# Performance work log

Measured on AMD Instinct MI355X. Metric: run time of the kernel, lower is better.

## Reference

```python
import jax, jax.numpy as jnp
import numpy as np

B, S, D, H = 4, 2048, 1024, 16
DH = D // H


def setup_inputs() -> dict:
    key = jax.random.key(0)
    k1, k2, k3, k4, k5 = jax.random.split(key, 5)
    X = jax.random.normal(k1, (B, S, D), dtype=jnp.float32)
    W1 = jax.random.normal(k2, (3 * D, D), dtype=jnp.float32) * 0.02
    b1 = jax.random.normal(k3, (3 * D,), dtype=jnp.float32) * 0.01
    W2 = jax.random.normal(k4, (D, D), dtype=jnp.float32) * 0.02
    b2 = jax.random.normal(k5, (D,), dtype=jnp.float32) * 0.01
    return {"X": X, "W1": W1, "b1": b1, "W2": W2, "b2": b2}


def reference(X, W1, b1, W2, b2):
    b, s, d = X.shape
    # fused QKV projection (nn.Linear: y = x @ W.T + b)
    Y = X @ W1.T + b1                                   # [B,S,3D]
    Q, K, V = jnp.split(Y, 3, axis=2)                   # each [B,S,D]
    # reshape(x): view (B,S,H,DH) then permute(0,2,3,1) -> [B,H,DH,S]
    q = Q.reshape(b, s, H, DH).transpose(0, 2, 3, 1)    # [B,H,DH,S]
    v = V.reshape(b, s, H, DH).transpose(0, 2, 3, 1)    # [B,H,DH,S]
    # reshape(x, k=True): permute(0,2,1,3) -> [B,H,S,DH]
    k = K.reshape(b, s, H, DH).transpose(0, 2, 1, 3)    # [B,H,S,DH]
    # w = q @ k / sqrt(q.size(-1)) ; note q.size(-1) == S in this layout
    w = jnp.einsum('bhds,bhse->bhde', q, k) / jnp.sqrt(jnp.asarray(s, X.dtype))  # [B,H,DH,DH]
    w = jax.nn.softmax(w, axis=-1)
    out = jnp.einsum('bhde,bhes->bhds', w, v)           # [B,H,DH,S]
    # cat(): raw contiguous view of [B,H,DH,S] into [B,S,H*DH] (memory-order reshape)
    out = out.reshape(b, s, H * DH)                     # [B,S,D]
    return out @ W2.T + b2
```

## Files before the change

### kernel.cpp

```cpp
#include <hip/hip_runtime.h>
#include <stdint.h>

#define B_ 4
#define S_ 2048
#define D_ 1024
#define H_ 16
#define DH_ 64
#define M_TOT (B_*S_)
#define N1_ (3*D_)
#define K_ D_
#define NCH 8

typedef __bf16 bf16_8 __attribute__((ext_vector_type(8)));
typedef float  f32x4  __attribute__((ext_vector_type(4)));
typedef unsigned short u16;

typedef __attribute__((address_space(1))) const void* gas_t;
typedef __attribute__((address_space(3))) void*       las_t;

__device__ __forceinline__ unsigned short f2bf(float f) {
    union { float f; unsigned u; } v; v.f = f;
    unsigned r = v.u + 0x7FFFu + ((v.u >> 16) & 1u);
    return (unsigned short)(r >> 16);
}

__device__ __forceinline__ void async_ld16(const void* g, void* l) {
    __builtin_amdgcn_global_load_lds((gas_t)g, (las_t)l, 16, 0, 0);
}

__global__ __launch_bounds__(256)
void cast_kernel(const float* __restrict__ X, const float* __restrict__ W1,
                 const float* __restrict__ W2, unsigned short* __restrict__ Xb,
                 unsigned short* __restrict__ W1b, unsigned short* __restrict__ W2b) {
    const int nX  = (M_TOT * K_) / 4;
    const int nW1 = (N1_ * K_) / 4;
    int i = blockIdx.x * 256 + threadIdx.x;
    const float4* src; unsigned short* dst; int j;
    if (i < nX)            { src = (const float4*)X;  dst = Xb;  j = i; }
    else if (i < nX + nW1) { src = (const float4*)W1; dst = W1b; j = i - nX; }
    else                   { src = (const float4*)W2; dst = W2b; j = i - nX - nW1; }
    float4 v = src[j];
    ushort4 o;
    o.x = f2bf(v.x); o.y = f2bf(v.y); o.z = f2bf(v.z); o.w = f2bf(v.w);
    ((ushort4*)dst)[j] = o;
}

template<int N, int NBX, bool OUT_BF16>
__global__ __launch_bounds__(256)
void gemm_bt(const unsigned short* __restrict__ A,
             const unsigned short* __restrict__ Bm,
             const float* __restrict__ bias,
             void* __restrict__ C, int K) {
    __shared__ unsigned short As[128 * 64];
    __shared__ unsigned short Bs[128 * 64];
    const int t    = threadIdx.x;
    const int wid  = t >> 6;
    const int lane = t & 63;
    const int lrow = lane & 15;
    const int lq   = lane >> 4;

    const int lid  = blockIdx.y * NBX + blockIdx.x;
    const int xcd  = lid & 7;
    const int slot = lid >> 3;
    const int by   = xcd * (gridDim.y >> 3) + slot / NBX;
    const int bx   = slot % NBX;
    const int m0   = by * 128;
    const int n0   = bx * 128;

    const int wm   = (wid >> 1) * 64;
    const int wn   = (wid & 1) * 64;

    f32x4 acc[4][4] = {};

    for (int k0 = 0; k0 < K; k0 += 64) {
#pragma unroll
        for (int p = 0; p < 4; p++) {
            const int c   = p * 256 + t;
            const int row = c >> 3;
            const int kb  = (c & 7) ^ (row & 7);
            async_ld16(A  + (size_t)(m0 + row) * K + k0 + kb * 8, (char*)As + c * 16);
            async_ld16(Bm + (size_t)(n0 + row) * K + k0 + kb * 8, (char*)Bs + c * 16);
        }
        __syncthreads();

#pragma unroll
        for (int ks = 0; ks < 2; ks++) {
            bf16_8 af[4], bfr[4];
#pragma unroll
            for (int mt = 0; mt < 4; mt++) {
                const int r  = wm + mt * 16 + lrow;
                const int kb = (ks * 4 + lq) ^ (r & 7);
                af[mt] = *(const bf16_8*)(As + (r * 8 + kb) * 8);
            }
#pragma unroll
            for (int nt = 0; nt < 4; nt++) {
                const int r  = wn + nt * 16 + lrow;
                const int kb = (ks * 4 + lq) ^ (r & 7);
                bfr[nt] = *(const bf16_8*)(Bs + (r * 8 + kb) * 8);
            }
#pragma unroll
            for (int mt = 0; mt < 4; mt++)
#pragma unroll
                for (int nt = 0; nt < 4; nt++)
                    acc[mt][nt] = __builtin_amdgcn_mfma_f32_16x16x32_bf16(af[mt], bfr[nt], acc[mt][nt], 0, 0, 0);
        }
        __syncthreads();
    }

#pragma unroll
    for (int nt = 0; nt < 4; nt++) {
        const int col = n0 + wn + nt * 16 + lrow;
        const float bv = bias[col];
#pragma unroll
        for (int mt = 0; mt < 4; mt++) {
            const int row = m0 + wm + mt * 16 + lq * 4;
            f32x4 a = acc[mt][nt];
            if (OUT_BF16) {
                unsigned short* Cp = (unsigned short*)C;
#pragma unroll
                for (int i = 0; i < 4; i++)
                    Cp[(size_t)(row + i) * N + col] = f2bf(a[i] + bv);
            } else {
                float* Cp = (float*)C;
#pragma unroll
                for (int i = 0; i < 4; i++)
                    Cp[(size_t)(row + i) * N + col] = a[i] + bv;
            }
        }
    }
}


#define LDA_H(AS, MH, AF) do {                                                     \
  _Pragma("unroll") for (int m_ = 0; m_ < 4; m_++)                                 \
  _Pragma("unroll") for (int ks_ = 0; ks_ < 2; ks_++) {                            \
    const int rho_ = (MH)*128 + wr*64 + m_*16 + lrow;                              \
    AF[m_][ks_] = *(const bf16_8*)((const u16*)(AS) + rho_*64 +                    \
                                   (((ks_*4+lq) ^ (lrow&7)) << 3)); } } while (0)

#define LDB_H(BS, NH, BF) do {                                                     \
  _Pragma("unroll") for (int n_ = 0; n_ < 2; n_++)                                 \
  _Pragma("unroll") for (int ks_ = 0; ks_ < 2; ks_++) {                            \
    const int rho_ = (NH)*128 + wc*32 + n_*16 + lrow;                              \
    BF[n_][ks_] = *(const bf16_8*)((const u16*)(BS) + rho_*64 +                    \
                                   (((ks_*4+lq) ^ (lrow&7)) << 3)); } } while (0)

#define MMA_Q(MH, NH, AF, BF) do {                                                 \
    __builtin_amdgcn_s_setprio(1);                                                 \
    _Pragma("unroll") for (int ks_ = 0; ks_ < 2; ks_++)                            \
    _Pragma("unroll") for (int m_ = 0; m_ < 4; m_++)                               \
    _Pragma("unroll") for (int n_ = 0; n_ < 2; n_++)                               \
        acc[(MH)*4+m_][(NH)*2+n_] = __builtin_amdgcn_mfma_f32_16x16x32_bf16(       \
            AF[m_][ks_], BF[n_][ks_], acc[(MH)*4+m_][(NH)*2+n_], 0, 0, 0);         \
    __builtin_amdgcn_s_setprio(0);                                                 \
  } while (0)

#define BAR()       __builtin_amdgcn_s_barrier()
#define WAIT_LGKM() do { asm volatile("s_waitcnt lgkmcnt(0)" ::: "memory");        \
                         __builtin_amdgcn_sched_barrier(0); } while (0)

template<int N, int NBX, int KK, bool OUT_BF16>
__global__ __launch_bounds__(512, 1)
void gemm_bt2(const u16* __restrict__ A, const u16* __restrict__ Bm,
              const float* __restrict__ bias, void* __restrict__ C) {
    __shared__ u16 As[2][256 * 64];
    __shared__ u16 Bs[2][256 * 64];

    const int t    = threadIdx.x;
    const int wid  = t >> 6;
    const int lane = t & 63;
    const int lrow = lane & 15;
    const int lq   = lane >> 4;
    const int wr   = wid >> 2;
    const int wc   = wid & 3;

    const int lid  = blockIdx.y * NBX + blockIdx.x;
    const int xcd  = lid & 7;
    const int slot = lid >> 3;
    const int by   = xcd * (gridDim.y >> 3) + slot / NBX;
    const int bx   = slot % NBX;
    const int m0   = by * 256;
    const int n0   = bx * 256;

    const u16* Ab = A  + (size_t)m0 * KK;
    const u16* Bb = Bm + (size_t)n0 * KK;

    f32x4 acc[8][4] = {};

    auto STG = [&](const u16* __restrict__ G, char* lds, int half, int k0, bool isA) {
#pragma unroll
        for (int cc = 0; cc < 2; cc++) {
            const int rho = half * 128 + cc * 64 + (t >> 3);
            const int blk = t & 7;
            const int g   = isA ? (((rho >> 6) & 1) * 128 + ((rho >> 7) & 1) * 64 + (rho & 63))
                                : (((rho >> 5) & 3) * 64  + ((rho >> 7) & 1) * 32 + (rho & 31));
            async_ld16(G + (size_t)g * KK + k0 + ((blk ^ (rho & 7)) << 3),
                       lds + rho * 128 + blk * 16);
        }
    };

    char* as0 = (char*)&As[0][0]; char* as1 = (char*)&As[1][0];
    char* bs0 = (char*)&Bs[0][0]; char* bs1 = (char*)&Bs[1][0];

    STG(Ab, as0, 0, 0,  true);
    STG(Bb, bs0, 0, 0,  false);
    STG(Bb, bs0, 1, 0,  false);
    STG(Ab, as0, 1, 0,  true);
    STG(Ab, as1, 0, 64, true);
    STG(Bb, bs1, 0, 64, false);
    STG(Bb, bs1, 1, 64, false);
    asm volatile("s_waitcnt vmcnt(6)" ::: "memory");
    BAR();

    bf16_8 af[4][2], blo[2][2], bhi[2][2];

    constexpr int NT = KK / 64;
    constexpr int NI = NT / 2;

    for (int i = 0; i < NI; ++i) {
        const bool pf = (i < NI - 1);
        const int kE = (2 * i + 2) * 64;
        const int kO = (2 * i + 3) * 64;

        LDA_H(as0, 0, af);
        LDB_H(bs0, 0, blo);
        STG(Ab, as1, 1, (2 * i + 1) * 64, true);
        BAR(); WAIT_LGKM();
        MMA_Q(0, 0, af, blo);
        BAR();
        LDB_H(bs0, 1, bhi);
        if (pf) STG(Ab, as0, 0, kE, true);
        BAR(); WAIT_LGKM();
        MMA_Q(0, 1, af, bhi);
        BAR();
        LDA_H(as0, 1, af);
        if (pf) STG(Bb, bs0, 0, kE, false);
        BAR(); WAIT_LGKM();
        MMA_Q(1, 1, af, bhi);
        BAR();
        if (pf) STG(Bb, bs0, 1, kE, false);
        BAR();
        MMA_Q(1, 0, af, blo);
        if (pf) { asm volatile("s_waitcnt vmcnt(6)" ::: "memory"); }
        else    { asm volatile("s_waitcnt vmcnt(0)" ::: "memory"); }
        BAR();
        LDA_H(as1, 0, af);
        LDB_H(bs1, 0, blo);
        if (pf) STG(Ab, as0, 1, kE, true);
        BAR(); WAIT_LGKM();
        MMA_Q(0, 0, af, blo);
        BAR();
        LDB_H(bs1, 1, bhi);
        if (pf) STG(Ab, as1, 0, kO, true);
        BAR(); WAIT_LGKM();
        MMA_Q(0, 1, af, bhi);
        BAR();
        LDA_H(as1, 1, af);
        if (pf) STG(Bb, bs1, 0, kO, false);
        BAR(); WAIT_LGKM();
        MMA_Q(1, 1, af, bhi);
        BAR();
        if (pf) STG(Bb, bs1, 1, kO, false);
        BAR();
        MMA_Q(1, 0, af, blo);
        if (pf) asm volatile("s_waitcnt vmcnt(6)" ::: "memory");
        BAR();
    }

#pragma unroll
    for (int nt = 0; nt < 4; nt++) {
        const int col = n0 + wc * 64 + nt * 16 + lrow;
        const float bv = bias[col];
#pragma unroll
        for (int mt = 0; mt < 8; mt++) {
            const int row = m0 + wr * 128 + mt * 16 + lq * 4;
            f32x4 a = acc[mt][nt];
            if (OUT_BF16) {
                u16* Cp = (u16*)C;
#pragma unroll
                for (int i2 = 0; i2 < 4; i2++)
                    Cp[(size_t)(row + i2) * N + col] = f2bf(a[i2] + bv);
            } else {
                float* Cp = (float*)C;
#pragma unroll
                for (int i2 = 0; i2 < 4; i2++)
                    Cp[(size_t)(row + i2) * N + col] = a[i2] + bv;
            }
        }
    }
}

__global__ __launch_bounds__(256)
void attn_scores(const unsigned short* __restrict__ Y, float* __restrict__ Scp) {
    __shared__ unsigned short Qs[64 * 72];
    __shared__ unsigned short Ks[64 * 72];
    const int bh = blockIdx.x, ch = blockIdx.y;
    const int b = bh >> 4, h = bh & 15;
    const size_t ybase = (size_t)b * S_ * 3072;
    const int qoff = h * 64, koff = D_ + h * 64;
    const int t = threadIdx.x, wid = t >> 6, lane = t & 63;
    const int lrow = lane & 15, lq = lane >> 4;

    f32x4 acc[4] = {};
    const int sbeg = ch * (S_ / NCH);
    for (int s0 = sbeg; s0 < sbeg + S_ / NCH; s0 += 64) {
#pragma unroll
        for (int p = 0; p < 4; p++) {
            int idx = p * 256 + t;
            int r = idx >> 4, cg = (idx & 15) * 4;
            const size_t gb = ybase + (size_t)(s0 + r) * 3072;
            ushort4 q4 = *(const ushort4*)(Y + gb + qoff + cg);
            ushort4 k4 = *(const ushort4*)(Y + gb + koff + cg);
            Qs[(cg + 0) * 72 + r] = q4.x; Qs[(cg + 1) * 72 + r] = q4.y;
            Qs[(cg + 2) * 72 + r] = q4.z; Qs[(cg + 3) * 72 + r] = q4.w;
            Ks[(cg + 0) * 72 + r] = k4.x; Ks[(cg + 1) * 72 + r] = k4.y;
            Ks[(cg + 2) * 72 + r] = k4.z; Ks[(cg + 3) * 72 + r] = k4.w;
        }
        __syncthreads();
#pragma unroll
        for (int ks = 0; ks < 2; ks++) {
            bf16_8 aq = *(const bf16_8*)(Qs + (wid * 16 + lrow) * 72 + ks * 32 + lq * 8);
#pragma unroll
            for (int nt = 0; nt < 4; nt++) {
                bf16_8 bk = *(const bf16_8*)(Ks + (nt * 16 + lrow) * 72 + ks * 32 + lq * 8);
                acc[nt] = __builtin_amdgcn_mfma_f32_16x16x32_bf16(aq, bk, acc[nt], 0, 0, 0);
            }
        }
        __syncthreads();
    }

    float* out = Scp + (size_t)(bh * NCH + ch) * 64 * 64;
#pragma unroll
    for (int nt = 0; nt < 4; nt++)
#pragma unroll
        for (int i = 0; i < 4; i++)
            out[(wid * 16 + lq * 4 + i) * 64 + nt * 16 + lrow] = acc[nt][i];
}

__global__ __launch_bounds__(256)
void attn_softmax(const float* __restrict__ Scp, unsigned short* __restrict__ Wb) {
    const int bh = blockIdx.x;
    const int t = threadIdx.x;
    const int d = t >> 2, q = t & 3;
    float s[16] = {};
#pragma unroll
    for (int c = 0; c < NCH; c++) {
        const float4* p = (const float4*)(Scp + ((size_t)(bh * NCH + c) * 64 + d) * 64 + q * 16);
#pragma unroll
        for (int j = 0; j < 4; j++) {
            float4 v = p[j];
            s[j*4+0] += v.x; s[j*4+1] += v.y; s[j*4+2] += v.z; s[j*4+3] += v.w;
        }
    }
    const float scale = 0.022097086912079608f;
    float m = -3.0e38f;
#pragma unroll
    for (int i = 0; i < 16; i++) { s[i] *= scale; m = fmaxf(m, s[i]); }
    m = fmaxf(m, __shfl_xor(m, 1));
    m = fmaxf(m, __shfl_xor(m, 2));
    float sum = 0.f;
#pragma unroll
    for (int i = 0; i < 16; i++) { s[i] = __expf(s[i] - m); sum += s[i]; }
    sum += __shfl_xor(sum, 1);
    sum += __shfl_xor(sum, 2);
    const float inv = 1.0f / sum;
    unsigned short* w = Wb + (size_t)bh * 4096 + d * 64 + q * 16;
    ushort4 o0, o1, o2, o3;
    o0.x=f2bf(s[0]*inv);  o0.y=f2bf(s[1]*inv);  o0.z=f2bf(s[2]*inv);  o0.w=f2bf(s[3]*inv);
    o1.x=f2bf(s[4]*inv);  o1.y=f2bf(s[5]*inv);  o1.z=f2bf(s[6]*inv);  o1.w=f2bf(s[7]*inv);
    o2.x=f2bf(s[8]*inv);  o2.y=f2bf(s[9]*inv);  o2.z=f2bf(s[10]*inv); o2.w=f2bf(s[11]*inv);
    o3.x=f2bf(s[12]*inv); o3.y=f2bf(s[13]*inv); o3.z=f2bf(s[14]*inv); o3.w=f2bf(s[15]*inv);
    ((ushort4*)w)[0]=o0; ((ushort4*)w)[1]=o1; ((ushort4*)w)[2]=o2; ((ushort4*)w)[3]=o3;
}

__global__ __launch_bounds__(256)
void attn_out(const unsigned short* __restrict__ Y, const unsigned short* __restrict__ Wb,
              unsigned short* __restrict__ O) {
    __shared__ unsigned short Ws[64 * 72];
    const int bh = blockIdx.x, sc = blockIdx.y;
    const int b = bh >> 4, h = bh & 15;
    const size_t ybase = (size_t)b * S_ * 3072;
    const int voff = 2 * D_ + h * 64;
    const int t = threadIdx.x, wid = t >> 6, lane = t & 63;
    const int lrow = lane & 15, lq = lane >> 4;

    {
        const int d = t >> 2, q = t & 3;
        const uint4* src = (const uint4*)(Wb + (size_t)bh * 4096 + d * 64 + q * 16);
        uint4* dst = (uint4*)(Ws + d * 72 + q * 16);
        dst[0] = src[0];
        *(uint4*)(Ws + d * 72 + q * 16 + 8) = src[1];
    }
    __syncthreads();

    bf16_8 aw[4][2];
#pragma unroll
    for (int mt = 0; mt < 4; mt++)
#pragma unroll
        for (int ks = 0; ks < 2; ks++)
            aw[mt][ks] = *(const bf16_8*)(Ws + (mt * 16 + lrow) * 72 + ks * 32 + lq * 8);

    const size_t obase = (size_t)b * (H_ * DH_ * S_) + (size_t)h * (DH_ * S_);
    const int s0 = sc * 256 + wid * 64;
    f32x4 o[4][4] = {};
#pragma unroll
    for (int ks = 0; ks < 2; ks++) {
        bf16_8 bv[4];
#pragma unroll
        for (int nt = 0; nt < 4; nt++)
            bv[nt] = *(const bf16_8*)(Y + ybase + (size_t)(s0 + nt * 16 + lrow) * 3072 + voff + ks * 32 + lq * 8);
#pragma unroll
        for (int mt = 0; mt < 4; mt++)
#pragma unroll
            for (int nt = 0; nt < 4; nt++)
                o[mt][nt] = __builtin_amdgcn_mfma_f32_16x16x32_bf16(aw[mt][ks], bv[nt], o[mt][nt], 0, 0, 0);
    }
#pragma unroll
    for (int mt = 0; mt < 4; mt++)
#pragma unroll
        for (int nt = 0; nt < 4; nt++) {
            const int d = mt * 16 + lq * 4;
            const int s = s0 + nt * 16 + lrow;
#pragma unroll
            for (int i = 0; i < 4; i++)
                O[obase + (size_t)(d + i) * S_ + s] = f2bf(o[mt][nt][i]);
        }
}

extern "C" void kernel_launch(void* const* d_in, const int* in_sizes, int n_in,
                              void* d_out, int out_size, void* d_ws, size_t ws_size,
                              hipStream_t stream) {
    const float* X  = (const float*)d_in[0];
    const float* W1 = (const float*)d_in[1];
    const float* b1 = (const float*)d_in[2];
    const float* W2 = (const float*)d_in[3];
    const float* b2 = (const float*)d_in[4];

    char* ws = (char*)d_ws;
    unsigned short* Xb  = (unsigned short*)(ws + 0);
    unsigned short* W1b = (unsigned short*)(ws + (16u << 20));
    unsigned short* W2b = (unsigned short*)(ws + (22u << 20));
    unsigned short* Yb  = (unsigned short*)(ws + (24u << 20));
    unsigned short* Wb  = (unsigned short*)(ws + 0);
    unsigned short* Ob  = (unsigned short*)(ws + (1u << 20));
    float* Scp = (float*)d_out;

    cast_kernel<<<12288, 256, 0, stream>>>(X, W1, W2, Xb, W1b, W2b);
    gemm_bt2<N1_, N1_/256, K_, true><<<dim3(N1_ / 256, M_TOT / 256), 512, 0, stream>>>(Xb, W1b, b1, Yb);
    attn_scores<<<dim3(64, NCH), 256, 0, stream>>>(Yb, Scp);
    attn_softmax<<<64, 256, 0, stream>>>(Scp, Wb);
    attn_out<<<dim3(64, NCH), 256, 0, stream>>>(Yb, Wb, Ob);
    gemm_bt<D_, D_/128, false><<<dim3(D_ / 128, M_TOT / 128), 256, 0, stream>>>(Ob, W2b, b2, d_out, K_);
}
```

Measured before the change: 221.9 us.

## Shrink QKV GEMM tile to 256x128 and fuse softmax into attention output

The QKV projection GEMM tile shrinks from 256x256 to 256x128. Each of 8 waves now owns a 64x64 sub-tile, the B staging buffer is halved, and the vmcnt waits are adjusted to match. This doubles the block count from 384 to 768 to fill the GPU's compute units better, at the cost of lower arithmetic intensity per block. Separately, the softmax kernel is fused into the attention-output kernel: each block recomputes the 64x64 softmax straight into shared memory. That removes one launch and the bf16 weight round-trip, but repeats the partial-score reduction across the 8 sequence chunks.

```diff
diff --git a/kernel.cpp b/kernel.cpp
--- a/kernel.cpp
+++ b/kernel.cpp
@@ -132,26 +132,26 @@
 
 
 #define LDA_H(AS, MH, AF) do {                                                     \
-  _Pragma("unroll") for (int m_ = 0; m_ < 4; m_++)                                 \
+  _Pragma("unroll") for (int m_ = 0; m_ < 2; m_++)                                 \
   _Pragma("unroll") for (int ks_ = 0; ks_ < 2; ks_++) {                            \
-    const int rho_ = (MH)*128 + wr*64 + m_*16 + lrow;                              \
+    const int rho_ = (MH)*128 + wr*32 + m_*16 + lrow;                              \
     AF[m_][ks_] = *(const bf16_8*)((const u16*)(AS) + rho_*64 +                    \
                                    (((ks_*4+lq) ^ (lrow&7)) << 3)); } } while (0)
 
 #define LDB_H(BS, NH, BF) do {                                                     \
   _Pragma("unroll") for (int n_ = 0; n_ < 2; n_++)                                 \
   _Pragma("unroll") for (int ks_ = 0; ks_ < 2; ks_++) {                            \
-    const int rho_ = (NH)*128 + wc*32 + n_*16 + lrow;                              \
+    const int rho_ = (NH)*64 + wc*32 + n_*16 + lrow;                               \
     BF[n_][ks_] = *(const bf16_8*)((const u16*)(BS) + rho_*64 +                    \
                                    (((ks_*4+lq) ^ (lrow&7)) << 3)); } } while (0)
 
 #define MMA_Q(MH, NH, AF, BF) do {                                                 \
     __builtin_amdgcn_s_setprio(1);                                                 \
     _Pragma("unroll") for (int ks_ = 0; ks_ < 2; ks_++)                            \
-    _Pragma("unroll") for (int m_ = 0; m_ < 4; m_++)                               \
+    _Pragma("unroll") for (int m_ = 0; m_ < 2; m_++)                               \
     _Pragma("unroll") for (int n_ = 0; n_ < 2; n_++)                               \
-        acc[(MH)*4+m_][(NH)*2+n_] = __builtin_amdgcn_mfma_f32_16x16x32_bf16(       \
-            AF[m_][ks_], BF[n_][ks_], acc[(MH)*4+m_][(NH)*2+n_], 0, 0, 0);         \
+        acc[(MH)*2+m_][(NH)*2+n_] = __builtin_amdgcn_mfma_f32_16x16x32_bf16(       \
+            AF[m_][ks_], BF[n_][ks_], acc[(MH)*2+m_][(NH)*2+n_], 0, 0, 0);         \
     __builtin_amdgcn_s_setprio(0);                                                 \
   } while (0)
 
@@ -161,18 +161,18 @@
 
 template<int N, int NBX, int KK, bool OUT_BF16>
 __global__ __launch_bounds__(512, 1)
-void gemm_bt2(const u16* __restrict__ A, const u16* __restrict__ Bm,
+void gemm_bt3(const u16* __restrict__ A, const u16* __restrict__ Bm,
               const float* __restrict__ bias, void* __restrict__ C) {
     __shared__ u16 As[2][256 * 64];
-    __shared__ u16 Bs[2][256 * 64];
+    __shared__ u16 Bs[2][128 * 64];
 
     const int t    = threadIdx.x;
     const int wid  = t >> 6;
     const int lane = t & 63;
     const int lrow = lane & 15;
     const int lq   = lane >> 4;
-    const int wr   = wid >> 2;
-    const int wc   = wid & 3;
+    const int wr   = wid >> 1;
+    const int wc   = wid & 1;
 
     const int lid  = blockIdx.y * NBX + blockIdx.x;
     const int xcd  = lid & 7;
@@ -180,39 +180,45 @@
     const int by   = xcd * (gridDim.y >> 3) + slot / NBX;
     const int bx   = slot % NBX;
     const int m0   = by * 256;
-    const int n0   = bx * 256;
+    const int n0   = bx * 128;
 
     const u16* Ab = A  + (size_t)m0 * KK;
     const u16* Bb = Bm + (size_t)n0 * KK;
 
-    f32x4 acc[8][4] = {};
-
-    auto STG = [&](const u16* __restrict__ G, char* lds, int half, int k0, bool isA) {
+    f32x4 acc[4][4] = {};
+
+    auto STGA = [&](char* lds, int half, int k0) {
 #pragma unroll
         for (int cc = 0; cc < 2; cc++) {
             const int rho = half * 128 + cc * 64 + (t >> 3);
             const int blk = t & 7;
-            const int g   = isA ? (((rho >> 6) & 1) * 128 + ((rho >> 7) & 1) * 64 + (rho & 63))
-                                : (((rho >> 5) & 3) * 64  + ((rho >> 7) & 1) * 32 + (rho & 31));
-            async_ld16(G + (size_t)g * KK + k0 + ((blk ^ (rho & 7)) << 3),
+            const int g   = ((rho >> 5) & 3) * 64 + (rho >> 7) * 32 + (rho & 31);
+            async_ld16(Ab + (size_t)g * KK + k0 + ((blk ^ (rho & 7)) << 3),
                        lds + rho * 128 + blk * 16);
         }
+    };
+    auto STGB = [&](char* lds, int half, int k0) {
+        const int rho = half * 64 + (t >> 3);
+        const int blk = t & 7;
+        const int g   = ((rho >> 5) & 1) * 64 + (rho >> 6) * 32 + (rho & 31);
+        async_ld16(Bb + (size_t)g * KK + k0 + ((blk ^ (rho & 7)) << 3),
+                   lds + rho * 128 + blk * 16);
     };
 
     char* as0 = (char*)&As[0][0]; char* as1 = (char*)&As[1][0];
     char* bs0 = (char*)&Bs[0][0]; char* bs1 = (char*)&Bs[1][0];
 
-    STG(Ab, as0, 0, 0,  true);
-    STG(Bb, bs0, 0, 0,  false);
-    STG(Bb, bs0, 1, 0,  false);
-    STG(Ab, as0, 1, 0,  true);
-    STG(Ab, as1, 0, 64, true);
-    STG(Bb, bs1, 0, 64, false);
-    STG(Bb, bs1, 1, 64, false);
-    asm volatile("s_waitcnt vmcnt(6)" ::: "memory");
+    STGA(as0, 0, 0);
+    STGB(bs0, 0, 0);
+    STGB(bs0, 1, 0);
+    STGA(as0, 1, 0);
+    STGA(as1, 0, 64);
+    STGB(bs1, 0, 64);
+    STGB(bs1, 1, 64);
+    asm volatile("s_waitcnt vmcnt(4)" ::: "memory");
     BAR();
 
-    bf16_8 af[4][2], blo[2][2], bhi[2][2];
+    bf16_8 af[2][2], blo[2][2], bhi[2][2];
 
     constexpr int NT = KK / 64;
     constexpr int NI = NT / 2;
@@ -224,46 +230,46 @@
 
         LDA_H(as0, 0, af);
         LDB_H(bs0, 0, blo);
-        STG(Ab, as1, 1, (2 * i + 1) * 64, true);
+        STGA(as1, 1, (2 * i + 1) * 64);
         BAR(); WAIT_LGKM();
         MMA_Q(0, 0, af, blo);
         BAR();
         LDB_H(bs0, 1, bhi);
-        if (pf) STG(Ab, as0, 0, kE, true);
+        if (pf) STGA(as0, 0, kE);
         BAR(); WAIT_LGKM();
         MMA_Q(0, 1, af, bhi);
         BAR();
         LDA_H(as0, 1, af);
-        if (pf) STG(Bb, bs0, 0, kE, false);
+        if (pf) STGB(bs0, 0, kE);
         BAR(); WAIT_LGKM();
         MMA_Q(1, 1, af, bhi);
         BAR();
-        if (pf) STG(Bb, bs0, 1, kE, false);
+        if (pf) STGB(bs0, 1, kE);
         BAR();
         MMA_Q(1, 0, af, blo);
-        if (pf) { asm volatile("s_waitcnt vmcnt(6)" ::: "memory"); }
+        if (pf) { asm volatile("s_waitcnt vmcnt(4)" ::: "memory"); }
         else    { asm volatile("s_waitcnt vmcnt(0)" ::: "memory"); }
         BAR();
         LDA_H(as1, 0, af);
         LDB_H(bs1, 0, blo);
-        if (pf) STG(Ab, as0, 1, kE, true);
+        if (pf) STGA(as0, 1, kE);
         BAR(); WAIT_LGKM();
         MMA_Q(0, 0, af, blo);
         BAR();
         LDB_H(bs1, 1, bhi);
-        if (pf) STG(Ab, as1, 0, kO, true);
+        if (pf) STGA(as1, 0, kO);
         BAR(); WAIT_LGKM();
         MMA_Q(0, 1, af, bhi);
         BAR();
         LDA_H(as1, 1, af);
-        if (pf) STG(Bb, bs1, 0, kO, false);
+        if (pf) STGB(bs1, 0, kO);
         BAR(); WAIT_LGKM();
         MMA_Q(1, 1, af, bhi);
         BAR();
-        if (pf) STG(Bb, bs1, 1, kO, false);
+        if (pf) STGB(bs1, 1, kO);
         BAR();
         MMA_Q(1, 0, af, blo);
-        if (pf) asm volatile("s_waitcnt vmcnt(6)" ::: "memory");
+        if (pf) asm volatile("s_waitcnt vmcnt(4)" ::: "memory");
         BAR();
     }
 
@@ -272,8 +278,8 @@
         const int col = n0 + wc * 64 + nt * 16 + lrow;
         const float bv = bias[col];
 #pragma unroll
-        for (int mt = 0; mt < 8; mt++) {
-            const int row = m0 + wr * 128 + mt * 16 + lq * 4;
+        for (int mt = 0; mt < 4; mt++) {
+            const int row = m0 + wr * 64 + mt * 16 + lq * 4;
             f32x4 a = acc[mt][nt];
             if (OUT_BF16) {
                 u16* Cp = (u16*)C;
@@ -338,44 +344,9 @@
 }
 
 __global__ __launch_bounds__(256)
-void attn_softmax(const float* __restrict__ Scp, unsigned short* __restrict__ Wb) {
-    const int bh = blockIdx.x;
-    const int t = threadIdx.x;
-    const int d = t >> 2, q = t & 3;
-    float s[16] = {};
-#pragma unroll
-    for (int c = 0; c < NCH; c++) {
-        const float4* p = (const float4*)(Scp + ((size_t)(bh * NCH + c) * 64 + d) * 64 + q * 16);
-#pragma unroll
-        for (int j = 0; j < 4; j++) {
-            float4 v = p[j];
-            s[j*4+0] += v.x; s[j*4+1] += v.y; s[j*4+2] += v.z; s[j*4+3] += v.w;
-        }
-    }
-    const float scale = 0.022097086912079608f;
-    float m = -3.0e38f;
-#pragma unroll
-    for (int i = 0; i < 16; i++) { s[i] *= scale; m = fmaxf(m, s[i]); }
-    m = fmaxf(m, __shfl_xor(m, 1));
-    m = fmaxf(m, __shfl_xor(m, 2));
-    float sum = 0.f;
-#pragma unroll
-    for (int i = 0; i < 16; i++) { s[i] = __expf(s[i] - m); sum += s[i]; }
-    sum += __shfl_xor(sum, 1);
-    sum += __shfl_xor(sum, 2);
-    const float inv = 1.0f / sum;
-    unsigned short* w = Wb + (size_t)bh * 4096 + d * 64 + q * 16;
-    ushort4 o0, o1, o2, o3;
-    o0.x=f2bf(s[0]*inv);  o0.y=f2bf(s[1]*inv);  o0.z=f2bf(s[2]*inv);  o0.w=f2bf(s[3]*inv);
-    o1.x=f2bf(s[4]*inv);  o1.y=f2bf(s[5]*inv);  o1.z=f2bf(s[6]*inv);  o1.w=f2bf(s[7]*inv);
-    o2.x=f2bf(s[8]*inv);  o2.y=f2bf(s[9]*inv);  o2.z=f2bf(s[10]*inv); o2.w=f2bf(s[11]*inv);
-    o3.x=f2bf(s[12]*inv); o3.y=f2bf(s[13]*inv); o3.z=f2bf(s[14]*inv); o3.w=f2bf(s[15]*inv);
-    ((ushort4*)w)[0]=o0; ((ushort4*)w)[1]=o1; ((ushort4*)w)[2]=o2; ((ushort4*)w)[3]=o3;
-}
-
-__global__ __launch_bounds__(256)
-void attn_out(const unsigned short* __restrict__ Y, const unsigned short* __restrict__ Wb,
-              unsigned short* __restrict__ O) {
+void attn_out_fused(const unsigned short* __restrict__ Y,
+                    const float* __restrict__ Scp,
+                    unsigned short* __restrict__ O) {
     __shared__ unsigned short Ws[64 * 72];
     const int bh = blockIdx.x, sc = blockIdx.y;
     const int b = bh >> 4, h = bh & 15;
@@ -386,10 +357,31 @@
 
     {
         const int d = t >> 2, q = t & 3;
-        const uint4* src = (const uint4*)(Wb + (size_t)bh * 4096 + d * 64 + q * 16);
-        uint4* dst = (uint4*)(Ws + d * 72 + q * 16);
-        dst[0] = src[0];
-        *(uint4*)(Ws + d * 72 + q * 16 + 8) = src[1];
+        float s[16] = {};
+#pragma unroll
+        for (int c = 0; c < NCH; c++) {
+            const float4* p = (const float4*)(Scp + ((size_t)(bh * NCH + c) * 64 + d) * 64 + q * 16);
+#pragma unroll
+            for (int j = 0; j < 4; j++) {
+                float4 v = p[j];
+                s[j*4+0] += v.x; s[j*4+1] += v.y; s[j*4+2] += v.z; s[j*4+3] += v.w;
+            }
+        }
+        const float scale = 0.022097086912079608f;
+        float m = -3.0e38f;
+#pragma unroll
+        for (int i = 0; i < 16; i++) { s[i] *= scale; m = fmaxf(m, s[i]); }
+        m = fmaxf(m, __shfl_xor(m, 1));
+        m = fmaxf(m, __shfl_xor(m, 2));
+        float sum = 0.f;
+#pragma unroll
+        for (int i = 0; i < 16; i++) { s[i] = __expf(s[i] - m); sum += s[i]; }
+        sum += __shfl_xor(sum, 1);
+        sum += __shfl_xor(sum, 2);
+        const float inv = 1.0f / sum;
+        unsigned short* w = Ws + d * 72 + q * 16;
+#pragma unroll
+        for (int i = 0; i < 16; i++) w[i] = f2bf(s[i] * inv);
     }
     __syncthreads();
 
@@ -441,14 +433,12 @@
     unsigned short* W1b = (unsigned short*)(ws + (16u << 20));
     unsigned short* W2b = (unsigned short*)(ws + (22u << 20));
     unsigned short* Yb  = (unsigned short*)(ws + (24u << 20));
-    unsigned short* Wb  = (unsigned short*)(ws + 0);
     unsigned short* Ob  = (unsigned short*)(ws + (1u << 20));
     float* Scp = (float*)d_out;
 
     cast_kernel<<<12288, 256, 0, stream>>>(X, W1, W2, Xb, W1b, W2b);
-    gemm_bt2<N1_, N1_/256, K_, true><<<dim3(N1_ / 256, M_TOT / 256), 512, 0, stream>>>(Xb, W1b, b1, Yb);
+    gemm_bt3<N1_, N1_/128, K_, true><<<dim3(N1_ / 128, M_TOT / 256), 512, 0, stream>>>(Xb, W1b, b1, Yb);
     attn_scores<<<dim3(64, NCH), 256, 0, stream>>>(Yb, Scp);
-    attn_softmax<<<64, 256, 0, stream>>>(Scp, Wb);
-    attn_out<<<dim3(64, NCH), 256, 0, stream>>>(Yb, Wb, Ob);
+    attn_out_fused<<<dim3(64, NCH), 256, 0, stream>>>(Yb, Scp, Ob);
     gemm_bt<D_, D_/128, false><<<dim3(D_ / 128, M_TOT / 128), 256, 0, stream>>>(Ob, W2b, b2, d_out, K_);
 }
```

Measured after the change: 216.8 us. -2.3%, faster.
